# Performance work log

Measured on AMD Instinct MI355X. Metric: run time of the kernel, lower is better.

## Reference

```python
import jax, jax.numpy as jnp
import numpy as np

N, CIN, COUT, V, T, S = 32, 64, 128, 25, 300, 3  # batch, in/out channels, joints, frames, subsets
EPS = 1e-5  # torch BatchNorm2d default eps


def setup_inputs() -> dict:
    key = jax.random.key(0)
    ks = jax.random.split(key, 16)
    f = lambda i, shape, sc=1.0: jax.random.normal(ks[i], shape, jnp.float32) * sc
    return dict(
        x=f(0, (N, CIN, V, T)),            # forward arg: input features
        ada_A=f(1, (N, CIN, V, V), 0.1),   # forward arg: adaptive adjacency features
        PA=f(2, (S, V, V), 0.1),           # learned adjacency (adaptive=True)
        conv3_w=f(3, (S, COUT, CIN), 0.05),  # per-subset 1x1 conv weights
        conv3_b=f(4, (S, COUT), 0.01),
        ada_w=f(5, (S, COUT, CIN), 0.05),    # per-subset conv_ada weights
        ada_b=f(6, (S, COUT), 0.01),
        bn_gamma=jnp.ones((COUT,), jnp.float32),
        bn_beta=jnp.zeros((COUT,), jnp.float32),
        bn_mean=f(7, (COUT,), 0.01),
        bn_var=jnp.abs(f(8, (COUT,))) + 1.0,
        down_w=f(9, (COUT, CIN), 0.05),      # residual 1x1 conv (in_c != out_c)
        down_b=f(10, (COUT,), 0.01),
        dbn_gamma=jnp.ones((COUT,), jnp.float32),
        dbn_beta=jnp.zeros((COUT,), jnp.float32),
        dbn_mean=f(11, (COUT,), 0.01),
        dbn_var=jnp.abs(f(12, (COUT,))) + 1.0,
    )


def _bn(y, g, b, m, v):
    # inference-mode BatchNorm2d over channel axis 1; y: [N, C, V, T]
    scale = g * jax.lax.rsqrt(v + EPS)
    return (y - m[:, None, None]) * scale[:, None, None] + b[:, None, None]


def reference(x, ada_A, PA, conv3_w, conv3_b, ada_w, ada_b,
              bn_gamma, bn_beta, bn_mean, bn_var,
              down_w, down_b, dbn_gamma, dbn_beta, dbn_mean, dbn_var):
    # per-subset 1x1 conv on features: feat[s] = conv3_s(x)  -> [S, N, COUT, V, T]
    feat = jnp.einsum('nivt,soi->snovt', x, conv3_w) + conv3_b[:, None, :, None, None]
    # per-subset 1x1 conv on adjacency features -> [S, N, COUT, V, V]
    adaA = jnp.einsum('nivw,soi->snovw', ada_A, ada_w) + ada_b[:, None, :, None, None]
    # modulate by learned adjacency PA[s] broadcast over (batch, channel)
    A_full = adaA * PA[:, None, None, :, :]
    # graph matmul per subset + sum over subsets -> [N, COUT, V, T]
    out = jnp.einsum('snovw,snowt->novt', A_full, feat)
    out = _bn(out, bn_gamma, bn_beta, bn_mean, bn_var)
    # residual down-path: 1x1 conv + BN (in_c != out_c)
    res = jnp.einsum('nivt,oi->novt', x, down_w) + down_b[:, None, None]
    res = _bn(res, dbn_gamma, dbn_beta, dbn_mean, dbn_var)
    return jax.nn.relu(out + res)
```

## Files before the change

kernel.cpp:

```cpp
#include <hip/hip_runtime.h>
#include <stdint.h>

#define N_    32
#define CIN_  64
#define COUT_ 128
#define V_    25
#define T_    300
#define S_    3


using short8 = __attribute__((ext_vector_type(8))) short;
using f32x4  = __attribute__((ext_vector_type(4))) float;

#define MFMA(a, b, c) __builtin_amdgcn_mfma_f32_16x16x32_bf16(a, b, c, 0, 0, 0)

#define OC  8
#define TC  32

__device__ __forceinline__ float b2f(unsigned short u) {
  return __uint_as_float(((uint32_t)u) << 16);
}
__device__ __forceinline__ unsigned short f2b(float f) {
  uint32_t u = __float_as_uint(f);
  u += 0x7fffu + ((u >> 16) & 1u);
  return (unsigned short)(u >> 16);
}
template<bool ISB>
__device__ __forceinline__ float ldf(const void* p, int i) {
  return ISB ? b2f(((const unsigned short*)p)[i]) : ((const float*)p)[i];
}
__device__ __forceinline__ short8 zero8() {
  short8 z = {0, 0, 0, 0, 0, 0, 0, 0};
  return z;
}
__device__ __forceinline__ short8 ld_s8(const unsigned short* p, int st) {
  union { uint32_t u[4]; short8 s; } r;
  r.u[0] = (uint32_t)p[0]      | ((uint32_t)p[st]     << 16);
  r.u[1] = (uint32_t)p[2 * st] | ((uint32_t)p[3 * st] << 16);
  r.u[2] = (uint32_t)p[4 * st] | ((uint32_t)p[5 * st] << 16);
  r.u[3] = (uint32_t)p[6 * st] | ((uint32_t)p[7 * st] << 16);
  return r.s;
}
__device__ __forceinline__ short8 ld_f8h(const float* p, int st) {
  short8 r;
#pragma unroll
  for (int j = 0; j < 8; ++j) r[j] = (short)f2b(p[j * st]);
  return r;
}
__device__ __forceinline__ void ld_f8s(const float* p, int st,
                                       short8& h, short8& l) {
#pragma unroll
  for (int j = 0; j < 8; ++j) {
    float xv = p[j * st];
    uint32_t u = __float_as_uint(xv);
    h[j] = (short)(u >> 16);
    l[j] = (short)f2b(xv - __uint_as_float(u & 0xffff0000u));
  }
}

__global__ void gcn_dtype_flag(const void* __restrict__ gamma, int* __restrict__ flag) {
  if (threadIdx.x == 0 && blockIdx.x == 0)
    flag[0] = (((const unsigned short*)gamma)[0] == 0x3F80u) ? 1 : 0;
}

template<bool ISB>
__global__ __launch_bounds__(256) void gcn_mfma(
    const void* __restrict__ x,    const void* __restrict__ ada,
    const void* __restrict__ PA,
    const void* __restrict__ c3w,  const void* __restrict__ c3b,
    const void* __restrict__ adw,  const void* __restrict__ adb,
    const void* __restrict__ bng,  const void* __restrict__ bnb,
    const void* __restrict__ bnm,  const void* __restrict__ bnv,
    const void* __restrict__ dww,  const void* __restrict__ dwb,
    const void* __restrict__ dbg,  const void* __restrict__ dbb,
    const void* __restrict__ dbm,  const void* __restrict__ dbv,
    void* __restrict__ out,
    const int* __restrict__ flag)
{
  if (ISB) { if (flag && flag[0] == 0) return; }
  else     { if (!flag || flag[0] != 0) return; }

  __shared__ __align__(16) unsigned char SM[74752];
  unsigned short* A_l = (unsigned short*)SM;
  float* resl = (float*)(SM + 49152);

  const int tid  = threadIdx.x;
  const int lane = tid & 63;
  const int tl   = lane & 15;
  const int khi  = lane >> 4;
  const int wv   = tid >> 6;

  const int b  = blockIdx.x;
  const int q  = b >> 3;
  const int n  = (b & 7) * 4 + (q >> 4);
  const int o0 = (q & 15) * OC;

  const unsigned short* xnu   = (const unsigned short*)x   + (size_t)n * (CIN_ * V_ * T_);
  const float*          xnf   = (const float*)x            + (size_t)n * (CIN_ * V_ * T_);
  const unsigned short* adanu = (const unsigned short*)ada + (size_t)n * (CIN_ * V_ * V_);
  const float*          adanf = (const float*)ada          + (size_t)n * (CIN_ * V_ * V_);

  float sc8[OC];
#pragma unroll
  for (int o = 0; o < OC; ++o)
    sc8[o] = ldf<ISB>(bng, o0 + o) * rsqrtf(ldf<ISB>(bnv, o0 + o) + 1e-5f);

  const int oA = wv * 2, oB = wv * 2 + 1;
  const float dscA = ldf<ISB>(dbg, o0 + oA) * rsqrtf(ldf<ISB>(dbv, o0 + oA) + 1e-5f);
  const float dscB = ldf<ISB>(dbg, o0 + oB) * rsqrtf(ldf<ISB>(dbv, o0 + oB) + 1e-5f);
  const float c0A  = ldf<ISB>(bnb, o0 + oA) + ldf<ISB>(dbb, o0 + oA)
                   - ldf<ISB>(bnm, o0 + oA) * sc8[oA] - ldf<ISB>(dbm, o0 + oA) * dscA;
  const float c0B  = ldf<ISB>(bnb, o0 + oB) + ldf<ISB>(dbb, o0 + oB)
                   - ldf<ISB>(bnm, o0 + oB) * sc8[oB] - ldf<ISB>(dbm, o0 + oB) * dscB;

  const int r0 = tl;
  const int r1 = 16 + tl;
  short8 wb00, wb01, wb10, wb11;
  short8 wb00l = zero8(), wb01l = zero8(), wb10l = zero8(), wb11l = zero8();
  if constexpr (ISB) {
    const unsigned short* wrow0 = (const unsigned short*)c3w
        + ((r0 >> 3) * COUT_ + o0 + (r0 & 7)) * CIN_;
    const unsigned short* wrow1 = (r1 < 24)
        ? (const unsigned short*)c3w + (2 * COUT_ + o0 + (r1 & 7)) * CIN_
        : (const unsigned short*)dww + (o0 + (r1 & 7)) * CIN_;
    wb00 = *(const short8*)(wrow0 + khi * 8);
    wb01 = *(const short8*)(wrow0 + 32 + khi * 8);
    wb10 = *(const short8*)(wrow1 + khi * 8);
    wb11 = *(const short8*)(wrow1 + 32 + khi * 8);
  } else {
    const float* wrow0 = (const float*)c3w
        + ((r0 >> 3) * COUT_ + o0 + (r0 & 7)) * CIN_;
    const float* wrow1 = (r1 < 24)
        ? (const float*)c3w + (2 * COUT_ + o0 + (r1 & 7)) * CIN_
        : (const float*)dww + (o0 + (r1 & 7)) * CIN_;
    ld_f8s(wrow0 + khi * 8,      1, wb00, wb00l);
    ld_f8s(wrow0 + 32 + khi * 8, 1, wb01, wb01l);
    ld_f8s(wrow1 + khi * 8,      1, wb10, wb10l);
    ld_f8s(wrow1 + 32 + khi * 8, 1, wb11, wb11l);
  }

  f32x4 fb0, fb1;
#pragma unroll
  for (int rg = 0; rg < 4; ++rg) {
    const int ra = khi * 4 + rg;
    fb0[rg] = ldf<ISB>(c3b, (ra >> 3) * COUT_ + o0 + (ra & 7));
    const int rb = 16 + ra;
    fb1[rg] = (rb < 24) ? ldf<ISB>(c3b, 2 * COUT_ + o0 + (rb & 7))
                        : ldf<ISB>(dwb, o0 + (rb & 7));
  }

  for (int e = tid; e < 12288; e += 256) ((float*)SM)[e] = 0.f;
  __syncthreads();

  {
    short8 aw00, aw01, aw10, aw11;
    if constexpr (ISB) {
      const unsigned short* arow0 = (const unsigned short*)adw
          + ((r0 >> 3) * COUT_ + o0 + (r0 & 7)) * CIN_;
      const unsigned short* arow1 = (const unsigned short*)adw
          + (2 * COUT_ + o0 + (tl & 7)) * CIN_;
      aw00 = *(const short8*)(arow0 + khi * 8);
      aw01 = *(const short8*)(arow0 + 32 + khi * 8);
      aw10 = (tl < 8) ? *(const short8*)(arow1 + khi * 8)      : zero8();
      aw11 = (tl < 8) ? *(const short8*)(arow1 + 32 + khi * 8) : zero8();
    } else {
      const float* arow0 = (const float*)adw
          + ((r0 >> 3) * COUT_ + o0 + (r0 & 7)) * CIN_;
      const float* arow1 = (const float*)adw
          + (2 * COUT_ + o0 + (tl & 7)) * CIN_;
      aw00 = ld_f8h(arow0 + khi * 8, 1);
      aw01 = ld_f8h(arow0 + 32 + khi * 8, 1);
      aw10 = (tl < 8) ? ld_f8h(arow1 + khi * 8, 1)      : zero8();
      aw11 = (tl < 8) ? ld_f8h(arow1 + 32 + khi * 8, 1) : zero8();
    }
    f32x4 ab0, ab1;
#pragma unroll
    for (int rg = 0; rg < 4; ++rg) {
      const int ra = khi * 4 + rg;
      ab0[rg] = ldf<ISB>(adb, (ra >> 3) * COUT_ + o0 + (ra & 7));
      const int rb = 16 + ra;
      ab1[rg] = (rb < 24) ? ldf<ISB>(adb, 2 * COUT_ + o0 + (rb & 7)) : 0.f;
    }

    for (int nt = wv * 10; nt < wv * 10 + 10; ++nt) {
      const int pos = nt * 16 + tl;
      const bool pv = pos < V_ * V_;
      short8 bf0 = zero8(), bf1 = zero8();
      if (pv) {
        if constexpr (ISB) {
          bf0 = ld_s8(adanu + (khi * 8) * 625 + pos, 625);
          bf1 = ld_s8(adanu + (32 + khi * 8) * 625 + pos, 625);
        } else {
          bf0 = ld_f8h(adanf + (khi * 8) * 625 + pos, 625);
          bf1 = ld_f8h(adanf + (32 + khi * 8) * 625 + pos, 625);
        }
      }
      f32x4 a0 = ab0, a1 = ab1;
      a0 = MFMA(aw00, bf0, a0);
      a0 = MFMA(aw01, bf1, a0);
      a1 = MFMA(aw10, bf0, a1);
      a1 = MFMA(aw11, bf1, a1);
      if (pv) {
        const int vv = pos / 25, ww = pos % 25;
        const float pa0 = ldf<ISB>(PA, pos);
        const float pa1 = ldf<ISB>(PA, 625 + pos);
        const float pa2 = ldf<ISB>(PA, 1250 + pos);
#pragma unroll
        for (int rg = 0; rg < 4; ++rg) {
          const int ra = khi * 4 + rg;
          const float pa = (ra >> 3) ? pa1 : pa0;
          A_l[(((ra & 7) * 3 + (ra >> 3)) * 32 + vv) * 32 + ww] =
              f2b(a0[rg] * pa * sc8[ra & 7]);
          const int rb = 16 + ra;
          if (rb < 24)
            A_l[(((rb & 7) * 3 + 2) * 32 + vv) * 32 + ww] =
                f2b(a1[rg] * pa2 * sc8[rb & 7]);
        }
      }
    }
  }
  __syncthreads();

  short8 afr[2][3][2];
#pragma unroll
  for (int oc = 0; oc < 2; ++oc) {
    const int oo = wv * 2 + oc;
#pragma unroll
    for (int s = 0; s < 3; ++s)
#pragma unroll
      for (int mt = 0; mt < 2; ++mt)
        afr[oc][s][mt] = *(const short8*)(
            A_l + (((oo * 3 + s) * 32 + mt * 16 + tl) * 32 + khi * 8));
  }
  __syncthreads();

  for (int e = tid; e < 12288; e += 256) ((float*)SM)[e] = 0.f;
  __syncthreads();

  const int wlo = (wv == 0) ? 0 : 1 + 6 * wv;
  const int whi = 7 + 6 * wv;

  for (int ch = 0; ch < 10; ++ch) {
    const int t0 = ch * TC;

    for (int w = wlo; w < whi; ++w) {
#pragma unroll
      for (int nt = 0; nt < 2; ++nt) {
        const int tt = t0 + nt * 16;
        if (tt < T_) {
          const int t = tt + tl;
          f32x4 f0 = fb0, f1 = fb1;
          if constexpr (ISB) {
            short8 xf0 = zero8(), xf1 = zero8();
            if (t < T_) {
              const unsigned short* xp = xnu + (khi * 8) * (V_ * T_) + w * T_ + t;
              xf0 = ld_s8(xp, V_ * T_);
              xf1 = ld_s8(xp + 32 * (V_ * T_), V_ * T_);
            }
            f0 = MFMA(wb00, xf0, f0);
            f0 = MFMA(wb01, xf1, f0);
            f1 = MFMA(wb10, xf0, f1);
            f1 = MFMA(wb11, xf1, f1);
          } else {
            short8 xh0 = zero8(), xl0 = zero8(), xh1 = zero8(), xl1 = zero8();
            if (t < T_) {
              const float* xp = xnf + (khi * 8) * (V_ * T_) + w * T_ + t;
              ld_f8s(xp, V_ * T_, xh0, xl0);
              ld_f8s(xp + 32 * (V_ * T_), V_ * T_, xh1, xl1);
            }
            f32x4 g0 = {0.f, 0.f, 0.f, 0.f}, g1 = {0.f, 0.f, 0.f, 0.f};
            f0 = MFMA(wb00, xh0, f0);
            f0 = MFMA(wb01, xh1, f0);
            f1 = MFMA(wb10, xh0, f1);
            f1 = MFMA(wb11, xh1, f1);
            g0 = MFMA(wb00, xl0, g0);
            g0 = MFMA(wb01, xl1, g0);
            g0 = MFMA(wb00l, xh0, g0);
            g0 = MFMA(wb01l, xh1, g0);
            g1 = MFMA(wb10, xl0, g1);
            g1 = MFMA(wb11, xl1, g1);
            g1 = MFMA(wb10l, xh0, g1);
            g1 = MFMA(wb11l, xh1, g1);
            f0 = f0 + g0;
            f1 = f1 + g1;
          }
          const int tlc = nt * 16 + tl;
          const unsigned sw = (unsigned)(w * 2) ^ ((unsigned)(tlc & 3) << 4);
#pragma unroll
          for (int rg = 0; rg < 4; ++rg) {
            const int ra = khi * 4 + rg;
            *(unsigned short*)(SM + (ra * TC + tlc) * 64 + sw) = f2b(f0[rg]);
            const int rb = 16 + ra;
            if (rb < 24)
              *(unsigned short*)(SM + (rb * TC + tlc) * 64 + sw) = f2b(f1[rg]);
            else
              resl[((rb - 24) * V_ + w) * TC + tlc] = f1[rg];
          }
        }
      }
    }
    __syncthreads();

#pragma unroll
    for (int oc = 0; oc < 2; ++oc) {
      const int oo  = wv * 2 + oc;
      const float dsc = oc ? dscB : dscA;
      const float c0v = oc ? c0B : c0A;
#pragma unroll
      for (int nt = 0; nt < 2; ++nt) {
        const int tt = t0 + nt * 16;
        if (tt < T_) {
          const int tlc = nt * 16 + tl;
          const unsigned rsw = (unsigned)(khi ^ (tlc & 3)) << 4;
          f32x4 d0 = {0.f, 0.f, 0.f, 0.f};
          f32x4 d1 = {0.f, 0.f, 0.f, 0.f};
#pragma unroll
          for (int s = 0; s < 3; ++s) {
            const short8 bf =
                *(const short8*)(SM + ((s * 8 + oo) * TC + tlc) * 64 + rsw);
            d0 = MFMA(afr[oc][s][0], bf, d0);
            d1 = MFMA(afr[oc][s][1], bf, d1);
          }
          const int t = tt + tl;
          if (t < T_) {
            const size_t obase = (size_t)(n * COUT_ + o0 + oo) * (V_ * T_) + t;
            unsigned short* opu = (unsigned short*)out + obase;
            float*          opf = (float*)out + obase;
#pragma unroll
            for (int rg = 0; rg < 4; ++rg) {
              const int v0 = khi * 4 + rg;
              const float y0 = fmaxf(
                  d0[rg] + resl[(oo * V_ + v0) * TC + tlc] * dsc + c0v, 0.f);
              if constexpr (ISB) opu[v0 * T_] = f2b(y0);
              else               opf[v0 * T_] = y0;
              const int v1 = 16 + v0;
              if (v1 < V_) {
                const float y1 = fmaxf(
                    d1[rg] + resl[(oo * V_ + v1) * TC + tlc] * dsc + c0v, 0.f);
                if constexpr (ISB) opu[v1 * T_] = f2b(y1);
                else               opf[v1 * T_] = y1;
              }
            }
          }
        }
      }
    }
    __syncthreads();
  }
}

extern "C" void kernel_launch(void* const* d_in, const int* in_sizes, int n_in,
                              void* d_out, int out_size, void* d_ws, size_t ws_size,
                              hipStream_t stream) {
  int* flag = (ws_size >= sizeof(int)) ? (int*)d_ws : nullptr;
  if (flag) gcn_dtype_flag<<<1, 64, 0, stream>>>(d_in[7], flag);

  gcn_mfma<true><<<dim3(512), 256, 0, stream>>>(
      d_in[0], d_in[1], d_in[2], d_in[3], d_in[4], d_in[5], d_in[6],
      d_in[7], d_in[8], d_in[9], d_in[10], d_in[11], d_in[12],
      d_in[13], d_in[14], d_in[15], d_in[16], d_out, flag);

  if (flag)
    gcn_mfma<false><<<dim3(512), 256, 0, stream>>>(
        d_in[0], d_in[1], d_in[2], d_in[3], d_in[4], d_in[5], d_in[6],
        d_in[7], d_in[8], d_in[9], d_in[10], d_in[11], d_in[12],
        d_in[13], d_in[14], d_in[15], d_in[16], d_out, flag);
}
```

Before: 453.2 us.

## Split time axis across blocks, shrink LDS, and prepack fp32 x into bf16 hi/lo pairs

Grid doubles to 1024 blocks, each covering half the time range in 16-frame chunks. This shrinks LDS from ~73KB to ~38KB and adds launch_bounds occupancy 4, so more blocks fit per CU. A new pack_x pre-pass converts fp32 x into packed bf16 hi/lo words in the workspace, so the main kernel loads one 32-bit word per element instead of splitting floats in-loop. The A buffer layout is trimmed to 25 rows with a new LDS swizzle. The trade-offs are that the graph-adjacency prologue is recomputed twice as often and the extra pack pass adds global traffic.

```diff
diff --git a/kernel.cpp b/kernel.cpp
--- a/kernel.cpp
+++ b/kernel.cpp
@@ -14,8 +14,8 @@
 
 #define MFMA(a, b, c) __builtin_amdgcn_mfma_f32_16x16x32_bf16(a, b, c, 0, 0, 0)
 
-#define OC  8
-#define TC  32
+#define OC   8
+#define TCH  16
 
 __device__ __forceinline__ float b2f(unsigned short u) {
   return __uint_as_float(((uint32_t)u) << 16);
@@ -57,14 +57,56 @@
     l[j] = (short)f2b(xv - __uint_as_float(u & 0xffff0000u));
   }
 }
+__device__ __forceinline__ void ld_pk8(const uint32_t* p, int st,
+                                       short8& h, short8& l) {
+  uint32_t a[8];
+#pragma unroll
+  for (int j = 0; j < 8; ++j) a[j] = p[j * st];
+  union { uint32_t u[4]; short8 s; } H, L;
+#pragma unroll
+  for (int k = 0; k < 4; ++k) {
+    H.u[k] = (a[2 * k] >> 16)      | (a[2 * k + 1] & 0xffff0000u);
+    L.u[k] = (a[2 * k] & 0xffffu)  | (a[2 * k + 1] << 16);
+  }
+  h = H.s; l = L.s;
+}
 
 __global__ void gcn_dtype_flag(const void* __restrict__ gamma, int* __restrict__ flag) {
   if (threadIdx.x == 0 && blockIdx.x == 0)
     flag[0] = (((const unsigned short*)gamma)[0] == 0x3F80u) ? 1 : 0;
 }
 
-template<bool ISB>
-__global__ __launch_bounds__(256) void gcn_mfma(
+__global__ __launch_bounds__(256) void pack_x(
+    const float* __restrict__ x, uint32_t* __restrict__ xp,
+    const int* __restrict__ flag) {
+  if (!flag || flag[0] != 0) return;
+  const int i = blockIdx.x * 256 + threadIdx.x;
+  const float4* s = (const float4*)x;
+  float4 a = s[2 * i], b = s[2 * i + 1];
+  uint4 o0, o1;
+  float av[4] = {a.x, a.y, a.z, a.w};
+  float bv[4] = {b.x, b.y, b.z, b.w};
+  uint32_t ou[8];
+#pragma unroll
+  for (int k = 0; k < 4; ++k) {
+    uint32_t u = __float_as_uint(av[k]);
+    uint32_t h = u & 0xffff0000u;
+    ou[k] = h | (uint32_t)f2b(av[k] - __uint_as_float(h));
+  }
+#pragma unroll
+  for (int k = 0; k < 4; ++k) {
+    uint32_t u = __float_as_uint(bv[k]);
+    uint32_t h = u & 0xffff0000u;
+    ou[4 + k] = h | (uint32_t)f2b(bv[k] - __uint_as_float(h));
+  }
+  o0.x = ou[0]; o0.y = ou[1]; o0.z = ou[2]; o0.w = ou[3];
+  o1.x = ou[4]; o1.y = ou[5]; o1.z = ou[6]; o1.w = ou[7];
+  ((uint4*)xp)[2 * i]     = o0;
+  ((uint4*)xp)[2 * i + 1] = o1;
+}
+
+template<bool ISB, bool PACK>
+__global__ __launch_bounds__(256, 4) void gcn_mfma(
     const void* __restrict__ x,    const void* __restrict__ ada,
     const void* __restrict__ PA,
     const void* __restrict__ c3w,  const void* __restrict__ c3b,
@@ -75,14 +117,15 @@
     const void* __restrict__ dbg,  const void* __restrict__ dbb,
     const void* __restrict__ dbm,  const void* __restrict__ dbv,
     void* __restrict__ out,
+    const uint32_t* __restrict__ xpk,
     const int* __restrict__ flag)
 {
   if (ISB) { if (flag && flag[0] == 0) return; }
   else     { if (!flag || flag[0] != 0) return; }
 
-  __shared__ __align__(16) unsigned char SM[74752];
+  __shared__ __align__(16) unsigned char SM[38400];
   unsigned short* A_l = (unsigned short*)SM;
-  float* resl = (float*)(SM + 49152);
+  float* resl = (float*)(SM + 24576);
 
   const int tid  = threadIdx.x;
   const int lane = tid & 63;
@@ -92,11 +135,15 @@
 
   const int b  = blockIdx.x;
   const int q  = b >> 3;
-  const int n  = (b & 7) * 4 + (q >> 4);
-  const int o0 = (q & 15) * OC;
+  const int n  = (b & 7) * 4 + (q >> 5);
+  const int o0 = ((q >> 1) & 15) * OC;
+  const int th = q & 1;
+  const int tbase = th ? 160 : 0;
+  const int nch   = th ? 9 : 10;
 
   const unsigned short* xnu   = (const unsigned short*)x   + (size_t)n * (CIN_ * V_ * T_);
   const float*          xnf   = (const float*)x            + (size_t)n * (CIN_ * V_ * T_);
+  const uint32_t*       xnq   = xpk                        + (size_t)n * (CIN_ * V_ * T_);
   const unsigned short* adanu = (const unsigned short*)ada + (size_t)n * (CIN_ * V_ * V_);
   const float*          adanf = (const float*)ada          + (size_t)n * (CIN_ * V_ * V_);
 
@@ -149,7 +196,7 @@
                         : ldf<ISB>(dwb, o0 + (rb & 7));
   }
 
-  for (int e = tid; e < 12288; e += 256) ((float*)SM)[e] = 0.f;
+  for (int e = tid; e < 9600; e += 256) ((float*)SM)[e] = 0.f;
   __syncthreads();
 
   {
@@ -209,11 +256,11 @@
         for (int rg = 0; rg < 4; ++rg) {
           const int ra = khi * 4 + rg;
           const float pa = (ra >> 3) ? pa1 : pa0;
-          A_l[(((ra & 7) * 3 + (ra >> 3)) * 32 + vv) * 32 + ww] =
+          A_l[(((ra & 7) * 3 + (ra >> 3)) * 25 + vv) * 32 + ww] =
               f2b(a0[rg] * pa * sc8[ra & 7]);
           const int rb = 16 + ra;
           if (rb < 24)
-            A_l[(((rb & 7) * 3 + 2) * 32 + vv) * 32 + ww] =
+            A_l[(((rb & 7) * 3 + 2) * 25 + vv) * 32 + ww] =
                 f2b(a1[rg] * pa2 * sc8[rb & 7]);
         }
       }
@@ -226,77 +273,77 @@
   for (int oc = 0; oc < 2; ++oc) {
     const int oo = wv * 2 + oc;
 #pragma unroll
-    for (int s = 0; s < 3; ++s)
-#pragma unroll
-      for (int mt = 0; mt < 2; ++mt)
-        afr[oc][s][mt] = *(const short8*)(
-            A_l + (((oo * 3 + s) * 32 + mt * 16 + tl) * 32 + khi * 8));
+    for (int s = 0; s < 3; ++s) {
+      afr[oc][s][0] = *(const short8*)(
+          A_l + (((oo * 3 + s) * 25 + tl) * 32 + khi * 8));
+      afr[oc][s][1] = (tl < 9)
+          ? *(const short8*)(A_l + (((oo * 3 + s) * 25 + 16 + tl) * 32 + khi * 8))
+          : zero8();
+    }
   }
   __syncthreads();
 
-  for (int e = tid; e < 12288; e += 256) ((float*)SM)[e] = 0.f;
+  for (int e = tid; e < 6144; e += 256) ((float*)SM)[e] = 0.f;
   __syncthreads();
 
   const int wlo = (wv == 0) ? 0 : 1 + 6 * wv;
   const int whi = 7 + 6 * wv;
 
-  for (int ch = 0; ch < 10; ++ch) {
-    const int t0 = ch * TC;
+  for (int ch = 0; ch < nch; ++ch) {
+    const int t  = tbase + ch * TCH + tl;
+    const bool tv = t < T_;
 
     for (int w = wlo; w < whi; ++w) {
-#pragma unroll
-      for (int nt = 0; nt < 2; ++nt) {
-        const int tt = t0 + nt * 16;
-        if (tt < T_) {
-          const int t = tt + tl;
-          f32x4 f0 = fb0, f1 = fb1;
-          if constexpr (ISB) {
-            short8 xf0 = zero8(), xf1 = zero8();
-            if (t < T_) {
-              const unsigned short* xp = xnu + (khi * 8) * (V_ * T_) + w * T_ + t;
-              xf0 = ld_s8(xp, V_ * T_);
-              xf1 = ld_s8(xp + 32 * (V_ * T_), V_ * T_);
-            }
-            f0 = MFMA(wb00, xf0, f0);
-            f0 = MFMA(wb01, xf1, f0);
-            f1 = MFMA(wb10, xf0, f1);
-            f1 = MFMA(wb11, xf1, f1);
+      f32x4 f0 = fb0, f1 = fb1;
+      if constexpr (ISB) {
+        short8 xf0 = zero8(), xf1 = zero8();
+        if (tv) {
+          const unsigned short* xp = xnu + (khi * 8) * (V_ * T_) + w * T_ + t;
+          xf0 = ld_s8(xp, V_ * T_);
+          xf1 = ld_s8(xp + 32 * (V_ * T_), V_ * T_);
+        }
+        f0 = MFMA(wb00, xf0, f0);
+        f0 = MFMA(wb01, xf1, f0);
+        f1 = MFMA(wb10, xf0, f1);
+        f1 = MFMA(wb11, xf1, f1);
+      } else {
+        short8 xh0 = zero8(), xl0 = zero8(), xh1 = zero8(), xl1 = zero8();
+        if (tv) {
+          const int off = (khi * 8) * (V_ * T_) + w * T_ + t;
+          if constexpr (PACK) {
+            ld_pk8(xnq + off, V_ * T_, xh0, xl0);
+            ld_pk8(xnq + off + 32 * (V_ * T_), V_ * T_, xh1, xl1);
           } else {
-            short8 xh0 = zero8(), xl0 = zero8(), xh1 = zero8(), xl1 = zero8();
-            if (t < T_) {
-              const float* xp = xnf + (khi * 8) * (V_ * T_) + w * T_ + t;
-              ld_f8s(xp, V_ * T_, xh0, xl0);
-              ld_f8s(xp + 32 * (V_ * T_), V_ * T_, xh1, xl1);
-            }
-            f32x4 g0 = {0.f, 0.f, 0.f, 0.f}, g1 = {0.f, 0.f, 0.f, 0.f};
-            f0 = MFMA(wb00, xh0, f0);
-            f0 = MFMA(wb01, xh1, f0);
-            f1 = MFMA(wb10, xh0, f1);
-            f1 = MFMA(wb11, xh1, f1);
-            g0 = MFMA(wb00, xl0, g0);
-            g0 = MFMA(wb01, xl1, g0);
-            g0 = MFMA(wb00l, xh0, g0);
-            g0 = MFMA(wb01l, xh1, g0);
-            g1 = MFMA(wb10, xl0, g1);
-            g1 = MFMA(wb11, xl1, g1);
-            g1 = MFMA(wb10l, xh0, g1);
-            g1 = MFMA(wb11l, xh1, g1);
-            f0 = f0 + g0;
-            f1 = f1 + g1;
-          }
-          const int tlc = nt * 16 + tl;
-          const unsigned sw = (unsigned)(w * 2) ^ ((unsigned)(tlc & 3) << 4);
-#pragma unroll
-          for (int rg = 0; rg < 4; ++rg) {
-            const int ra = khi * 4 + rg;
-            *(unsigned short*)(SM + (ra * TC + tlc) * 64 + sw) = f2b(f0[rg]);
-            const int rb = 16 + ra;
-            if (rb < 24)
-              *(unsigned short*)(SM + (rb * TC + tlc) * 64 + sw) = f2b(f1[rg]);
-            else
-              resl[((rb - 24) * V_ + w) * TC + tlc] = f1[rg];
+            ld_f8s(xnf + off, V_ * T_, xh0, xl0);
+            ld_f8s(xnf + off + 32 * (V_ * T_), V_ * T_, xh1, xl1);
           }
         }
+        f32x4 g0 = {0.f, 0.f, 0.f, 0.f}, g1 = {0.f, 0.f, 0.f, 0.f};
+        f0 = MFMA(wb00, xh0, f0);
+        f0 = MFMA(wb01, xh1, f0);
+        f1 = MFMA(wb10, xh0, f1);
+        f1 = MFMA(wb11, xh1, f1);
+        g0 = MFMA(wb00, xl0, g0);
+        g0 = MFMA(wb01, xl1, g0);
+        g0 = MFMA(wb00l, xh0, g0);
+        g0 = MFMA(wb01l, xh1, g0);
+        g1 = MFMA(wb10, xl0, g1);
+        g1 = MFMA(wb11, xl1, g1);
+        g1 = MFMA(wb10l, xh0, g1);
+        g1 = MFMA(wb11l, xh1, g1);
+        f0 = f0 + g0;
+        f1 = f1 + g1;
+      }
+      const int swb = ((((w >> 3) ^ (tl & 3) ^ khi) & 3) << 4) + (w & 7) * 2;
+#pragma unroll
+      for (int rg = 0; rg < 4; ++rg) {
+        const int ra = khi * 4 + rg;
+        *(unsigned short*)(SM + ra * 1024 + tl * 64 + swb) = f2b(f0[rg]);
+        const int rb = 16 + ra;
+        if (rb < 24)
+          *(unsigned short*)(SM + rb * 1024 + tl * 64 + swb) = f2b(f1[rg]);
+        else
+          resl[((khi * 4 + rg - 8) * 25 + w) * 16 + tl] = f1[rg];
       }
     }
     __syncthreads();
@@ -306,41 +353,34 @@
       const int oo  = wv * 2 + oc;
       const float dsc = oc ? dscB : dscA;
       const float c0v = oc ? c0B : c0A;
-#pragma unroll
-      for (int nt = 0; nt < 2; ++nt) {
-        const int tt = t0 + nt * 16;
-        if (tt < T_) {
-          const int tlc = nt * 16 + tl;
-          const unsigned rsw = (unsigned)(khi ^ (tlc & 3)) << 4;
-          f32x4 d0 = {0.f, 0.f, 0.f, 0.f};
-          f32x4 d1 = {0.f, 0.f, 0.f, 0.f};
-#pragma unroll
-          for (int s = 0; s < 3; ++s) {
-            const short8 bf =
-                *(const short8*)(SM + ((s * 8 + oo) * TC + tlc) * 64 + rsw);
-            d0 = MFMA(afr[oc][s][0], bf, d0);
-            d1 = MFMA(afr[oc][s][1], bf, d1);
-          }
-          const int t = tt + tl;
-          if (t < T_) {
-            const size_t obase = (size_t)(n * COUT_ + o0 + oo) * (V_ * T_) + t;
-            unsigned short* opu = (unsigned short*)out + obase;
-            float*          opf = (float*)out + obase;
-#pragma unroll
-            for (int rg = 0; rg < 4; ++rg) {
-              const int v0 = khi * 4 + rg;
-              const float y0 = fmaxf(
-                  d0[rg] + resl[(oo * V_ + v0) * TC + tlc] * dsc + c0v, 0.f);
-              if constexpr (ISB) opu[v0 * T_] = f2b(y0);
-              else               opf[v0 * T_] = y0;
-              const int v1 = 16 + v0;
-              if (v1 < V_) {
-                const float y1 = fmaxf(
-                    d1[rg] + resl[(oo * V_ + v1) * TC + tlc] * dsc + c0v, 0.f);
-                if constexpr (ISB) opu[v1 * T_] = f2b(y1);
-                else               opf[v1 * T_] = y1;
-              }
-            }
+      f32x4 d0 = {0.f, 0.f, 0.f, 0.f};
+      f32x4 d1 = {0.f, 0.f, 0.f, 0.f};
+#pragma unroll
+      for (int s = 0; s < 3; ++s) {
+        const int row = s * 8 + oo;
+        const short8 bf = *(const short8*)(
+            SM + row * 1024 + tl * 64
+               + (((khi ^ (tl & 3) ^ ((row >> 2) & 3)) & 3) << 4));
+        d0 = MFMA(afr[oc][s][0], bf, d0);
+        d1 = MFMA(afr[oc][s][1], bf, d1);
+      }
+      if (tv) {
+        const size_t obase = (size_t)(n * COUT_ + o0 + oo) * (V_ * T_) + t;
+        unsigned short* opu = (unsigned short*)out + obase;
+        float*          opf = (float*)out + obase;
+#pragma unroll
+        for (int rg = 0; rg < 4; ++rg) {
+          const int v0 = khi * 4 + rg;
+          const float y0 = fmaxf(
+              d0[rg] + resl[(oo * 25 + v0) * 16 + tl] * dsc + c0v, 0.f);
+          if constexpr (ISB) opu[v0 * T_] = f2b(y0);
+          else               opf[v0 * T_] = y0;
+          const int v1 = 16 + v0;
+          if (v1 < V_) {
+            const float y1 = fmaxf(
+                d1[rg] + resl[(oo * 25 + v1) * 16 + tl] * dsc + c0v, 0.f);
+            if constexpr (ISB) opu[v1 * T_] = f2b(y1);
+            else               opf[v1 * T_] = y1;
           }
         }
       }
@@ -352,17 +392,29 @@
 extern "C" void kernel_launch(void* const* d_in, const int* in_sizes, int n_in,
                               void* d_out, int out_size, void* d_ws, size_t ws_size,
                               hipStream_t stream) {
+  const size_t XPK_OFF   = 1024;
+  const size_t XPK_BYTES = (size_t)N_ * CIN_ * V_ * T_ * 4;
   int* flag = (ws_size >= sizeof(int)) ? (int*)d_ws : nullptr;
+  const bool ws_ok = flag && ws_size >= XPK_OFF + XPK_BYTES;
+  uint32_t* xpk = ws_ok ? (uint32_t*)((char*)d_ws + XPK_OFF) : nullptr;
+
   if (flag) gcn_dtype_flag<<<1, 64, 0, stream>>>(d_in[7], flag);
-
-  gcn_mfma<true><<<dim3(512), 256, 0, stream>>>(
+  if (ws_ok)
+    pack_x<<<dim3(7500), 256, 0, stream>>>((const float*)d_in[0], xpk, flag);
+
+  gcn_mfma<true, false><<<dim3(1024), 256, 0, stream>>>(
       d_in[0], d_in[1], d_in[2], d_in[3], d_in[4], d_in[5], d_in[6],
       d_in[7], d_in[8], d_in[9], d_in[10], d_in[11], d_in[12],
-      d_in[13], d_in[14], d_in[15], d_in[16], d_out, flag);
-
-  if (flag)
-    gcn_mfma<false><<<dim3(512), 256, 0, stream>>>(
+      d_in[13], d_in[14], d_in[15], d_in[16], d_out, nullptr, flag);
+
+  if (ws_ok)
+    gcn_mfma<false, true><<<dim3(1024), 256, 0, stream>>>(
         d_in[0], d_in[1], d_in[2], d_in[3], d_in[4], d_in[5], d_in[6],
         d_in[7], d_in[8], d_in[9], d_in[10], d_in[11], d_in[12],
-        d_in[13], d_in[14], d_in[15], d_in[16], d_out, flag);
-}
+        d_in[13], d_in[14], d_in[15], d_in[16], d_out, xpk, flag);
+  else if (flag)
+    gcn_mfma<false, false><<<dim3(1024), 256, 0, stream>>>(
+        d_in[0], d_in[1], d_in[2], d_in[3], d_in[4], d_in[5], d_in[6],
+        d_in[7], d_in[8], d_in[9], d_in[10], d_in[11], d_in[12],
+        d_in[13], d_in[14], d_in[15], d_in[16], d_out, nullptr, flag);
+}
```

Measured after the change: 479.4 us. +5.8%, slower.

## Pre-transpose x to channel-contiguous layout and halve per-block output channels

Applied to the files above, without the earlier changes.

Adds pre-pass kernels that transpose x into a [n][v][t][cin] bf16 layout in workspace (for fp32 input, split into hi/lo bf16 planes), so the main kernel can load MFMA B fragments with 16-byte vector loads instead of strided 2-byte gathers. The main kernel now handles 4 output channels per block over 1024 blocks with less shared memory and a 4-blocks-per-CU launch bound, and processes two joints per iteration in the bf16 path. This removes uncoalesced strided loads and raises occupancy, at the cost of an extra transpose pass and workspace traffic. The fp32 hi/lo split is changed to round-to-nearest.

```diff
diff --git a/kernel.cpp b/kernel.cpp
--- a/kernel.cpp
+++ b/kernel.cpp
@@ -13,9 +13,6 @@
 using f32x4  = __attribute__((ext_vector_type(4))) float;
 
 #define MFMA(a, b, c) __builtin_amdgcn_mfma_f32_16x16x32_bf16(a, b, c, 0, 0, 0)
-
-#define OC  8
-#define TC  32
 
 __device__ __forceinline__ float b2f(unsigned short u) {
   return __uint_as_float(((uint32_t)u) << 16);
@@ -52,9 +49,9 @@
 #pragma unroll
   for (int j = 0; j < 8; ++j) {
     float xv = p[j * st];
-    uint32_t u = __float_as_uint(xv);
-    h[j] = (short)(u >> 16);
-    l[j] = (short)f2b(xv - __uint_as_float(u & 0xffff0000u));
+    unsigned short hu = f2b(xv);
+    h[j] = (short)hu;
+    l[j] = (short)f2b(xv - b2f(hu));
   }
 }
 
@@ -63,8 +60,69 @@
     flag[0] = (((const unsigned short*)gamma)[0] == 0x3F80u) ? 1 : 0;
 }
 
-template<bool ISB>
-__global__ __launch_bounds__(256) void gcn_mfma(
+__global__ __launch_bounds__(256) void tx_bf(
+    const unsigned short* __restrict__ x, unsigned short* __restrict__ xt,
+    const int* __restrict__ flag) {
+  if (!flag || flag[0] == 0) return;
+  __shared__ uint32_t til[64][151];
+  const int b = blockIdx.x, n = b / 25, v = b % 25, tid = threadIdx.x;
+  const unsigned short* xp = x + (size_t)n * 480000 + v * 300;
+  for (int u = tid; u < 9600; u += 256) {
+    const int i = u / 150, tp = u % 150;
+    til[i][tp] = *(const uint32_t*)(xp + (size_t)i * 7500 + 2 * tp);
+  }
+  __syncthreads();
+  unsigned short* op = xt + (size_t)n * 480000 + (size_t)v * 19200;
+  for (int u = tid; u < 2400; u += 256) {
+    const int t = u >> 3, oct = u & 7;
+    uint32_t pk[4];
+#pragma unroll
+    for (int j = 0; j < 4; ++j) {
+      const uint32_t w0 = til[oct * 8 + 2 * j][t >> 1];
+      const uint32_t w1 = til[oct * 8 + 2 * j + 1][t >> 1];
+      const uint32_t a = (t & 1) ? (w0 >> 16) : (w0 & 0xffffu);
+      const uint32_t c = (t & 1) ? (w1 >> 16) : (w1 & 0xffffu);
+      pk[j] = a | (c << 16);
+    }
+    *(uint4*)(op + t * 64 + oct * 8) = *(uint4*)pk;
+  }
+}
+
+__global__ __launch_bounds__(256) void tx_f32(
+    const float* __restrict__ x, unsigned short* __restrict__ xh,
+    unsigned short* __restrict__ xl, const int* __restrict__ flag) {
+  if (!flag || flag[0] != 0) return;
+  __shared__ uint32_t til[64][303];
+  const int b = blockIdx.x, n = b / 25, v = b % 25, tid = threadIdx.x;
+  const float* xp = x + (size_t)n * 480000 + v * 300;
+  for (int u = tid; u < 9600; u += 256) {
+    const int i = u / 150, tp = u % 150;
+    const float2 xv = *(const float2*)(xp + (size_t)i * 7500 + 2 * tp);
+    unsigned short h0 = f2b(xv.x), h1 = f2b(xv.y);
+    unsigned short l0 = f2b(xv.x - b2f(h0)), l1 = f2b(xv.y - b2f(h1));
+    til[i][2 * tp]     = ((uint32_t)h0 << 16) | l0;
+    til[i][2 * tp + 1] = ((uint32_t)h1 << 16) | l1;
+  }
+  __syncthreads();
+  const size_t ob = (size_t)n * 480000 + (size_t)v * 19200;
+  for (int u = tid; u < 2400; u += 256) {
+    const int t = u >> 3, oct = u & 7;
+    uint32_t w[8];
+#pragma unroll
+    for (int k = 0; k < 8; ++k) w[k] = til[oct * 8 + k][t];
+    uint32_t ph[4], pl[4];
+#pragma unroll
+    for (int j = 0; j < 4; ++j) {
+      ph[j] = (w[2 * j] >> 16) | (w[2 * j + 1] & 0xffff0000u);
+      pl[j] = (w[2 * j] & 0xffffu) | (w[2 * j + 1] << 16);
+    }
+    *(uint4*)(xh + ob + t * 64 + oct * 8) = *(uint4*)ph;
+    *(uint4*)(xl + ob + t * 64 + oct * 8) = *(uint4*)pl;
+  }
+}
+
+template<bool ISB, bool TR>
+__global__ __launch_bounds__(256, 4) void gcn_mfma(
     const void* __restrict__ x,    const void* __restrict__ ada,
     const void* __restrict__ PA,
     const void* __restrict__ c3w,  const void* __restrict__ c3b,
@@ -75,14 +133,16 @@
     const void* __restrict__ dbg,  const void* __restrict__ dbb,
     const void* __restrict__ dbm,  const void* __restrict__ dbv,
     void* __restrict__ out,
+    const unsigned short* __restrict__ xt0,
+    const unsigned short* __restrict__ xt1,
     const int* __restrict__ flag)
 {
   if (ISB) { if (flag && flag[0] == 0) return; }
   else     { if (!flag || flag[0] != 0) return; }
 
-  __shared__ __align__(16) unsigned char SM[74752];
+  __shared__ __align__(16) unsigned char SM[37776];
   unsigned short* A_l = (unsigned short*)SM;
-  float* resl = (float*)(SM + 49152);
+  float* resl = (float*)(SM + 24576);
 
   const int tid  = threadIdx.x;
   const int lane = tid & 63;
@@ -91,100 +151,69 @@
   const int wv   = tid >> 6;
 
   const int b  = blockIdx.x;
-  const int q  = b >> 3;
-  const int n  = (b & 7) * 4 + (q >> 4);
-  const int o0 = (q & 15) * OC;
-
-  const unsigned short* xnu   = (const unsigned short*)x   + (size_t)n * (CIN_ * V_ * T_);
-  const float*          xnf   = (const float*)x            + (size_t)n * (CIN_ * V_ * T_);
-  const unsigned short* adanu = (const unsigned short*)ada + (size_t)n * (CIN_ * V_ * V_);
-  const float*          adanf = (const float*)ada          + (size_t)n * (CIN_ * V_ * V_);
-
-  float sc8[OC];
-#pragma unroll
-  for (int o = 0; o < OC; ++o)
-    sc8[o] = ldf<ISB>(bng, o0 + o) * rsqrtf(ldf<ISB>(bnv, o0 + o) + 1e-5f);
-
-  const int oA = wv * 2, oB = wv * 2 + 1;
-  const float dscA = ldf<ISB>(dbg, o0 + oA) * rsqrtf(ldf<ISB>(dbv, o0 + oA) + 1e-5f);
-  const float dscB = ldf<ISB>(dbg, o0 + oB) * rsqrtf(ldf<ISB>(dbv, o0 + oB) + 1e-5f);
-  const float c0A  = ldf<ISB>(bnb, o0 + oA) + ldf<ISB>(dbb, o0 + oA)
-                   - ldf<ISB>(bnm, o0 + oA) * sc8[oA] - ldf<ISB>(dbm, o0 + oA) * dscA;
-  const float c0B  = ldf<ISB>(bnb, o0 + oB) + ldf<ISB>(dbb, o0 + oB)
-                   - ldf<ISB>(bnm, o0 + oB) * sc8[oB] - ldf<ISB>(dbm, o0 + oB) * dscB;
-
-  const int r0 = tl;
-  const int r1 = 16 + tl;
-  short8 wb00, wb01, wb10, wb11;
-  short8 wb00l = zero8(), wb01l = zero8(), wb10l = zero8(), wb11l = zero8();
+  const int n  = (b & 7) * 4 + (b >> 8);
+  const int o0 = ((b >> 3) & 31) * 4;
+
+  const unsigned short* xnu   = (const unsigned short*)x   + (size_t)n * 480000;
+  const float*          xnf   = (const float*)x            + (size_t)n * 480000;
+  const unsigned short* adanu = (const unsigned short*)ada + (size_t)n * 40000;
+  const float*          adanf = (const float*)ada          + (size_t)n * 40000;
+  const unsigned short* xtn   = xt0 ? xt0 + (size_t)n * 480000 : nullptr;
+  const unsigned short* xln   = xt1 ? xt1 + (size_t)n * 480000 : nullptr;
+
+  float sc4[4];
+#pragma unroll
+  for (int o = 0; o < 4; ++o)
+    sc4[o] = ldf<ISB>(bng, o0 + o) * rsqrtf(ldf<ISB>(bnv, o0 + o) + 1e-5f);
+  const float dscv = ldf<ISB>(dbg, o0 + wv) * rsqrtf(ldf<ISB>(dbv, o0 + wv) + 1e-5f);
+  const float c0v  = ldf<ISB>(bnb, o0 + wv) + ldf<ISB>(dbb, o0 + wv)
+                   - ldf<ISB>(bnm, o0 + wv) * sc4[wv] - ldf<ISB>(dbm, o0 + wv) * dscv;
+
+  short8 wb0, wb1, wb0l = zero8(), wb1l = zero8();
   if constexpr (ISB) {
-    const unsigned short* wrow0 = (const unsigned short*)c3w
-        + ((r0 >> 3) * COUT_ + o0 + (r0 & 7)) * CIN_;
-    const unsigned short* wrow1 = (r1 < 24)
-        ? (const unsigned short*)c3w + (2 * COUT_ + o0 + (r1 & 7)) * CIN_
-        : (const unsigned short*)dww + (o0 + (r1 & 7)) * CIN_;
-    wb00 = *(const short8*)(wrow0 + khi * 8);
-    wb01 = *(const short8*)(wrow0 + 32 + khi * 8);
-    wb10 = *(const short8*)(wrow1 + khi * 8);
-    wb11 = *(const short8*)(wrow1 + 32 + khi * 8);
+    const unsigned short* wr = (tl < 12)
+        ? (const unsigned short*)c3w + ((tl >> 2) * COUT_ + o0 + (tl & 3)) * CIN_
+        : (const unsigned short*)dww + (o0 + (tl & 3)) * CIN_;
+    wb0 = *(const short8*)(wr + khi * 8);
+    wb1 = *(const short8*)(wr + 32 + khi * 8);
   } else {
-    const float* wrow0 = (const float*)c3w
-        + ((r0 >> 3) * COUT_ + o0 + (r0 & 7)) * CIN_;
-    const float* wrow1 = (r1 < 24)
-        ? (const float*)c3w + (2 * COUT_ + o0 + (r1 & 7)) * CIN_
-        : (const float*)dww + (o0 + (r1 & 7)) * CIN_;
-    ld_f8s(wrow0 + khi * 8,      1, wb00, wb00l);
-    ld_f8s(wrow0 + 32 + khi * 8, 1, wb01, wb01l);
-    ld_f8s(wrow1 + khi * 8,      1, wb10, wb10l);
-    ld_f8s(wrow1 + 32 + khi * 8, 1, wb11, wb11l);
-  }
-
-  f32x4 fb0, fb1;
-#pragma unroll
-  for (int rg = 0; rg < 4; ++rg) {
-    const int ra = khi * 4 + rg;
-    fb0[rg] = ldf<ISB>(c3b, (ra >> 3) * COUT_ + o0 + (ra & 7));
-    const int rb = 16 + ra;
-    fb1[rg] = (rb < 24) ? ldf<ISB>(c3b, 2 * COUT_ + o0 + (rb & 7))
-                        : ldf<ISB>(dwb, o0 + (rb & 7));
-  }
-
-  for (int e = tid; e < 12288; e += 256) ((float*)SM)[e] = 0.f;
-  __syncthreads();
-
+    const float* wr = (tl < 12)
+        ? (const float*)c3w + ((tl >> 2) * COUT_ + o0 + (tl & 3)) * CIN_
+        : (const float*)dww + (o0 + (tl & 3)) * CIN_;
+    ld_f8s(wr + khi * 8,      1, wb0, wb0l);
+    ld_f8s(wr + 32 + khi * 8, 1, wb1, wb1l);
+  }
+  f32x4 fbias;
+#pragma unroll
+  for (int rg = 0; rg < 4; ++rg)
+    fbias[rg] = (khi < 3) ? ldf<ISB>(c3b, khi * COUT_ + o0 + rg)
+                          : ldf<ISB>(dwb, o0 + rg);
+
+  for (int e = tid; e < 4800; e += 256) ((float*)SM)[e] = 0.f;
+  __syncthreads();
   {
-    short8 aw00, aw01, aw10, aw11;
-    if constexpr (ISB) {
-      const unsigned short* arow0 = (const unsigned short*)adw
-          + ((r0 >> 3) * COUT_ + o0 + (r0 & 7)) * CIN_;
-      const unsigned short* arow1 = (const unsigned short*)adw
-          + (2 * COUT_ + o0 + (tl & 7)) * CIN_;
-      aw00 = *(const short8*)(arow0 + khi * 8);
-      aw01 = *(const short8*)(arow0 + 32 + khi * 8);
-      aw10 = (tl < 8) ? *(const short8*)(arow1 + khi * 8)      : zero8();
-      aw11 = (tl < 8) ? *(const short8*)(arow1 + 32 + khi * 8) : zero8();
-    } else {
-      const float* arow0 = (const float*)adw
-          + ((r0 >> 3) * COUT_ + o0 + (r0 & 7)) * CIN_;
-      const float* arow1 = (const float*)adw
-          + (2 * COUT_ + o0 + (tl & 7)) * CIN_;
-      aw00 = ld_f8h(arow0 + khi * 8, 1);
-      aw01 = ld_f8h(arow0 + 32 + khi * 8, 1);
-      aw10 = (tl < 8) ? ld_f8h(arow1 + khi * 8, 1)      : zero8();
-      aw11 = (tl < 8) ? ld_f8h(arow1 + 32 + khi * 8, 1) : zero8();
-    }
-    f32x4 ab0, ab1;
-#pragma unroll
-    for (int rg = 0; rg < 4; ++rg) {
-      const int ra = khi * 4 + rg;
-      ab0[rg] = ldf<ISB>(adb, (ra >> 3) * COUT_ + o0 + (ra & 7));
-      const int rb = 16 + ra;
-      ab1[rg] = (rb < 24) ? ldf<ISB>(adb, 2 * COUT_ + o0 + (rb & 7)) : 0.f;
-    }
-
-    for (int nt = wv * 10; nt < wv * 10 + 10; ++nt) {
-      const int pos = nt * 16 + tl;
-      const bool pv = pos < V_ * V_;
+    short8 aw0 = zero8(), aw1 = zero8();
+    if (tl < 12) {
+      if constexpr (ISB) {
+        const unsigned short* ar = (const unsigned short*)adw
+            + ((tl >> 2) * COUT_ + o0 + (tl & 3)) * CIN_;
+        aw0 = *(const short8*)(ar + khi * 8);
+        aw1 = *(const short8*)(ar + 32 + khi * 8);
+      } else {
+        const float* ar = (const float*)adw
+            + ((tl >> 2) * COUT_ + o0 + (tl & 3)) * CIN_;
+        aw0 = ld_f8h(ar + khi * 8, 1);
+        aw1 = ld_f8h(ar + 32 + khi * 8, 1);
+      }
+    }
+    f32x4 ab;
+#pragma unroll
+    for (int rg = 0; rg < 4; ++rg)
+      ab[rg] = (khi < 3) ? ldf<ISB>(adb, khi * COUT_ + o0 + rg) : 0.f;
+
+    for (int ti = wv * 10; ti < wv * 10 + 10; ++ti) {
+      const int pos = ti * 16 + tl;
+      const bool pv = pos < 625;
       short8 bf0 = zero8(), bf1 = zero8();
       if (pv) {
         if constexpr (ISB) {
@@ -195,153 +224,167 @@
           bf1 = ld_f8h(adanf + (32 + khi * 8) * 625 + pos, 625);
         }
       }
-      f32x4 a0 = ab0, a1 = ab1;
-      a0 = MFMA(aw00, bf0, a0);
-      a0 = MFMA(aw01, bf1, a0);
-      a1 = MFMA(aw10, bf0, a1);
-      a1 = MFMA(aw11, bf1, a1);
-      if (pv) {
+      f32x4 acc = ab;
+      acc = MFMA(aw0, bf0, acc);
+      acc = MFMA(aw1, bf1, acc);
+      if (pv && khi < 3) {
         const int vv = pos / 25, ww = pos % 25;
-        const float pa0 = ldf<ISB>(PA, pos);
-        const float pa1 = ldf<ISB>(PA, 625 + pos);
-        const float pa2 = ldf<ISB>(PA, 1250 + pos);
-#pragma unroll
-        for (int rg = 0; rg < 4; ++rg) {
-          const int ra = khi * 4 + rg;
-          const float pa = (ra >> 3) ? pa1 : pa0;
-          A_l[(((ra & 7) * 3 + (ra >> 3)) * 32 + vv) * 32 + ww] =
-              f2b(a0[rg] * pa * sc8[ra & 7]);
-          const int rb = 16 + ra;
-          if (rb < 24)
-            A_l[(((rb & 7) * 3 + 2) * 32 + vv) * 32 + ww] =
-                f2b(a1[rg] * pa2 * sc8[rb & 7]);
-        }
-      }
-    }
-  }
-  __syncthreads();
-
-  short8 afr[2][3][2];
-#pragma unroll
-  for (int oc = 0; oc < 2; ++oc) {
-    const int oo = wv * 2 + oc;
-#pragma unroll
-    for (int s = 0; s < 3; ++s)
-#pragma unroll
-      for (int mt = 0; mt < 2; ++mt)
-        afr[oc][s][mt] = *(const short8*)(
-            A_l + (((oo * 3 + s) * 32 + mt * 16 + tl) * 32 + khi * 8));
-  }
-  __syncthreads();
-
-  for (int e = tid; e < 12288; e += 256) ((float*)SM)[e] = 0.f;
-  __syncthreads();
-
-  const int wlo = (wv == 0) ? 0 : 1 + 6 * wv;
-  const int whi = 7 + 6 * wv;
+        const float pa = ldf<ISB>(PA, khi * 625 + pos);
+#pragma unroll
+        for (int rg = 0; rg < 4; ++rg)
+          A_l[((rg * 3 + khi) * 25 + vv) * 32 + ww] = f2b(acc[rg] * pa * sc4[rg]);
+      }
+    }
+  }
+  __syncthreads();
+
+  short8 afr[3][2];
+#pragma unroll
+  for (int s = 0; s < 3; ++s) {
+    afr[s][0] = *(const short8*)(A_l + ((wv * 3 + s) * 25 + tl) * 32 + khi * 8);
+    afr[s][1] = (tl < 9)
+        ? *(const short8*)(A_l + ((wv * 3 + s) * 25 + 16 + tl) * 32 + khi * 8)
+        : zero8();
+  }
+  __syncthreads();
+
+  for (int e = tid; e < 6144; e += 256) ((float*)SM)[e] = 0.f;
+  __syncthreads();
+
+  const int wlo = wv * 6;
+  const int whi = (wv == 3) ? 25 : wv * 6 + 6;
 
   for (int ch = 0; ch < 10; ++ch) {
-    const int t0 = ch * TC;
-
-    for (int w = wlo; w < whi; ++w) {
-#pragma unroll
-      for (int nt = 0; nt < 2; ++nt) {
-        const int tt = t0 + nt * 16;
-        if (tt < T_) {
-          const int t = tt + tl;
-          f32x4 f0 = fb0, f1 = fb1;
-          if constexpr (ISB) {
-            short8 xf0 = zero8(), xf1 = zero8();
-            if (t < T_) {
-              const unsigned short* xp = xnu + (khi * 8) * (V_ * T_) + w * T_ + t;
-              xf0 = ld_s8(xp, V_ * T_);
-              xf1 = ld_s8(xp + 32 * (V_ * T_), V_ * T_);
-            }
-            f0 = MFMA(wb00, xf0, f0);
-            f0 = MFMA(wb01, xf1, f0);
-            f1 = MFMA(wb10, xf0, f1);
-            f1 = MFMA(wb11, xf1, f1);
-          } else {
-            short8 xh0 = zero8(), xl0 = zero8(), xh1 = zero8(), xl1 = zero8();
-            if (t < T_) {
-              const float* xp = xnf + (khi * 8) * (V_ * T_) + w * T_ + t;
-              ld_f8s(xp, V_ * T_, xh0, xl0);
-              ld_f8s(xp + 32 * (V_ * T_), V_ * T_, xh1, xl1);
-            }
-            f32x4 g0 = {0.f, 0.f, 0.f, 0.f}, g1 = {0.f, 0.f, 0.f, 0.f};
-            f0 = MFMA(wb00, xh0, f0);
-            f0 = MFMA(wb01, xh1, f0);
-            f1 = MFMA(wb10, xh0, f1);
-            f1 = MFMA(wb11, xh1, f1);
-            g0 = MFMA(wb00, xl0, g0);
-            g0 = MFMA(wb01, xl1, g0);
-            g0 = MFMA(wb00l, xh0, g0);
-            g0 = MFMA(wb01l, xh1, g0);
-            g1 = MFMA(wb10, xl0, g1);
-            g1 = MFMA(wb11, xl1, g1);
-            g1 = MFMA(wb10l, xh0, g1);
-            g1 = MFMA(wb11l, xh1, g1);
-            f0 = f0 + g0;
-            f1 = f1 + g1;
-          }
+    const int t0 = ch * 32;
+
+    if constexpr (ISB) {
+      for (int w = wlo; w < whi; w += 2) {
+        const bool pr = (w + 1 < whi);
+#pragma unroll
+        for (int nt = 0; nt < 2; ++nt) {
           const int tlc = nt * 16 + tl;
-          const unsigned sw = (unsigned)(w * 2) ^ ((unsigned)(tlc & 3) << 4);
-#pragma unroll
-          for (int rg = 0; rg < 4; ++rg) {
-            const int ra = khi * 4 + rg;
-            *(unsigned short*)(SM + (ra * TC + tlc) * 64 + sw) = f2b(f0[rg]);
-            const int rb = 16 + ra;
-            if (rb < 24)
-              *(unsigned short*)(SM + (rb * TC + tlc) * 64 + sw) = f2b(f1[rg]);
-            else
-              resl[((rb - 24) * V_ + w) * TC + tlc] = f1[rg];
-          }
-        }
-      }
-    }
-    __syncthreads();
-
-#pragma unroll
-    for (int oc = 0; oc < 2; ++oc) {
-      const int oo  = wv * 2 + oc;
-      const float dsc = oc ? dscB : dscA;
-      const float c0v = oc ? c0B : c0A;
-#pragma unroll
-      for (int nt = 0; nt < 2; ++nt) {
-        const int tt = t0 + nt * 16;
-        if (tt < T_) {
-          const int tlc = nt * 16 + tl;
-          const unsigned rsw = (unsigned)(khi ^ (tlc & 3)) << 4;
-          f32x4 d0 = {0.f, 0.f, 0.f, 0.f};
-          f32x4 d1 = {0.f, 0.f, 0.f, 0.f};
-#pragma unroll
-          for (int s = 0; s < 3; ++s) {
-            const short8 bf =
-                *(const short8*)(SM + ((s * 8 + oo) * TC + tlc) * 64 + rsw);
-            d0 = MFMA(afr[oc][s][0], bf, d0);
-            d1 = MFMA(afr[oc][s][1], bf, d1);
-          }
-          const int t = tt + tl;
-          if (t < T_) {
-            const size_t obase = (size_t)(n * COUT_ + o0 + oo) * (V_ * T_) + t;
-            unsigned short* opu = (unsigned short*)out + obase;
-            float*          opf = (float*)out + obase;
-#pragma unroll
-            for (int rg = 0; rg < 4; ++rg) {
-              const int v0 = khi * 4 + rg;
-              const float y0 = fmaxf(
-                  d0[rg] + resl[(oo * V_ + v0) * TC + tlc] * dsc + c0v, 0.f);
-              if constexpr (ISB) opu[v0 * T_] = f2b(y0);
-              else               opf[v0 * T_] = y0;
-              const int v1 = 16 + v0;
-              if (v1 < V_) {
-                const float y1 = fmaxf(
-                    d1[rg] + resl[(oo * V_ + v1) * TC + tlc] * dsc + c0v, 0.f);
-                if constexpr (ISB) opu[v1 * T_] = f2b(y1);
-                else               opf[v1 * T_] = y1;
+          const int t = t0 + tlc;
+          short8 a0 = zero8(), a1 = zero8(), b0 = zero8(), b1 = zero8();
+          if (t < 300) {
+            if constexpr (TR) {
+              const unsigned short* p = xtn + ((size_t)(w * 300 + t) << 6);
+              a0 = *(const short8*)(p + khi * 8);
+              a1 = *(const short8*)(p + 32 + khi * 8);
+              if (pr) {
+                b0 = *(const short8*)(p + 19200 + khi * 8);
+                b1 = *(const short8*)(p + 19200 + 32 + khi * 8);
+              }
+            } else {
+              const unsigned short* p = xnu + (khi * 8) * 7500 + w * 300 + t;
+              a0 = ld_s8(p, 7500);
+              a1 = ld_s8(p + 32 * 7500, 7500);
+              if (pr) {
+                b0 = ld_s8(p + 300, 7500);
+                b1 = ld_s8(p + 300 + 32 * 7500, 7500);
               }
             }
           }
+          f32x4 fA = fbias, fB = fbias;
+          fA = MFMA(wb0, a0, fA);
+          fA = MFMA(wb1, a1, fA);
+          fB = MFMA(wb0, b0, fB);
+          fB = MFMA(wb1, b1, fB);
+          if (khi == 3) {
+#pragma unroll
+            for (int rg = 0; rg < 4; ++rg) {
+              resl[(rg * 25 + w) * 33 + tlc] = fA[rg];
+              if (pr) resl[(rg * 25 + w + 1) * 33 + tlc] = fB[rg];
+            }
+          } else {
+            const int sb = ((((w >> 3) ^ (tl & 3) ^ khi) & 3) << 4) + (w & 7) * 2;
+            if (pr) {
+#pragma unroll
+              for (int rg = 0; rg < 4; ++rg)
+                *(uint32_t*)(SM + (khi * 4 + rg) * 2048 + tlc * 64 + sb)
+                    = (uint32_t)f2b(fA[rg]) | ((uint32_t)f2b(fB[rg]) << 16);
+            } else {
+#pragma unroll
+              for (int rg = 0; rg < 4; ++rg)
+                *(unsigned short*)(SM + (khi * 4 + rg) * 2048 + tlc * 64 + sb)
+                    = f2b(fA[rg]);
+            }
+          }
+        }
+      }
+    } else {
+      for (int w = wlo; w < whi; ++w) {
+#pragma unroll
+        for (int nt = 0; nt < 2; ++nt) {
+          const int tlc = nt * 16 + tl;
+          const int t = t0 + tlc;
+          short8 h0 = zero8(), h1 = zero8(), l0 = zero8(), l1 = zero8();
+          if (t < 300) {
+            if constexpr (TR) {
+              const size_t off = (size_t)(w * 300 + t) << 6;
+              h0 = *(const short8*)(xtn + off + khi * 8);
+              h1 = *(const short8*)(xtn + off + 32 + khi * 8);
+              l0 = *(const short8*)(xln + off + khi * 8);
+              l1 = *(const short8*)(xln + off + 32 + khi * 8);
+            } else {
+              const float* p = xnf + (khi * 8) * 7500 + w * 300 + t;
+              ld_f8s(p, 7500, h0, l0);
+              ld_f8s(p + 32 * 7500, 7500, h1, l1);
+            }
+          }
+          f32x4 f = fbias, g = {0.f, 0.f, 0.f, 0.f};
+          f = MFMA(wb0, h0, f);
+          f = MFMA(wb1, h1, f);
+          g = MFMA(wb0, l0, g);
+          g = MFMA(wb1, l1, g);
+          g = MFMA(wb0l, h0, g);
+          g = MFMA(wb1l, h1, g);
+          f = f + g;
+          if (khi == 3) {
+#pragma unroll
+            for (int rg = 0; rg < 4; ++rg)
+              resl[(rg * 25 + w) * 33 + tlc] = f[rg];
+          } else {
+            const int sb = ((((w >> 3) ^ (tl & 3) ^ khi) & 3) << 4) + (w & 7) * 2;
+#pragma unroll
+            for (int rg = 0; rg < 4; ++rg)
+              *(unsigned short*)(SM + (khi * 4 + rg) * 2048 + tlc * 64 + sb)
+                  = f2b(f[rg]);
+          }
+        }
+      }
+    }
+    __syncthreads();
+
+#pragma unroll
+    for (int nt = 0; nt < 2; ++nt) {
+      const int tlc = nt * 16 + tl;
+      const int t = t0 + tlc;
+      f32x4 d0 = {0.f, 0.f, 0.f, 0.f};
+      f32x4 d1 = {0.f, 0.f, 0.f, 0.f};
+#pragma unroll
+      for (int s = 0; s < 3; ++s) {
+        const int row = s * 4 + wv;
+        const short8 bf = *(const short8*)(
+            SM + row * 2048 + tlc * 64 + (((khi ^ (tlc & 3) ^ s) & 3) << 4));
+        d0 = MFMA(afr[s][0], bf, d0);
+        d1 = MFMA(afr[s][1], bf, d1);
+      }
+      if (t < 300) {
+        const int obase = (n * COUT_ + o0 + wv) * 7500 + t;
+#pragma unroll
+        for (int rg = 0; rg < 4; ++rg) {
+          const int v0 = khi * 4 + rg;
+          const float y0 = fmaxf(
+              d0[rg] + resl[(wv * 25 + v0) * 33 + tlc] * dscv + c0v, 0.f);
+          if constexpr (ISB) ((unsigned short*)out)[obase + v0 * 300] = f2b(y0);
+          else               ((float*)out)[obase + v0 * 300] = y0;
+          const int v1 = 16 + v0;
+          if (v1 < 25) {
+            const float y1 = fmaxf(
+                d1[rg] + resl[(wv * 25 + v1) * 33 + tlc] * dscv + c0v, 0.f);
+            if constexpr (ISB) ((unsigned short*)out)[obase + v1 * 300] = f2b(y1);
+            else               ((float*)out)[obase + v1 * 300] = y1;
+          }
         }
       }
     }
@@ -352,17 +395,40 @@
 extern "C" void kernel_launch(void* const* d_in, const int* in_sizes, int n_in,
                               void* d_out, int out_size, void* d_ws, size_t ws_size,
                               hipStream_t stream) {
+  const size_t PL = 30720000;
   int* flag = (ws_size >= sizeof(int)) ? (int*)d_ws : nullptr;
+  unsigned short* P0 = (unsigned short*)((char*)d_ws + 1024);
+  unsigned short* P1 = (unsigned short*)((char*)d_ws + 1024 + PL);
+  const bool trb = flag && ws_size >= 1024 + PL;
+  const bool trf = flag && ws_size >= 1024 + 2 * PL;
+
   if (flag) gcn_dtype_flag<<<1, 64, 0, stream>>>(d_in[7], flag);
-
-  gcn_mfma<true><<<dim3(512), 256, 0, stream>>>(
-      d_in[0], d_in[1], d_in[2], d_in[3], d_in[4], d_in[5], d_in[6],
-      d_in[7], d_in[8], d_in[9], d_in[10], d_in[11], d_in[12],
-      d_in[13], d_in[14], d_in[15], d_in[16], d_out, flag);
-
-  if (flag)
-    gcn_mfma<false><<<dim3(512), 256, 0, stream>>>(
+  if (trb) tx_bf<<<dim3(800), 256, 0, stream>>>(
+      (const unsigned short*)d_in[0], P0, flag);
+  if (trf) tx_f32<<<dim3(800), 256, 0, stream>>>(
+      (const float*)d_in[0], P0, P1, flag);
+
+  if (trb)
+    gcn_mfma<true, true><<<dim3(1024), 256, 0, stream>>>(
         d_in[0], d_in[1], d_in[2], d_in[3], d_in[4], d_in[5], d_in[6],
         d_in[7], d_in[8], d_in[9], d_in[10], d_in[11], d_in[12],
-        d_in[13], d_in[14], d_in[15], d_in[16], d_out, flag);
-}
+        d_in[13], d_in[14], d_in[15], d_in[16], d_out, P0, nullptr, flag);
+  else
+    gcn_mfma<true, false><<<dim3(1024), 256, 0, stream>>>(
+        d_in[0], d_in[1], d_in[2], d_in[3], d_in[4], d_in[5], d_in[6],
+        d_in[7], d_in[8], d_in[9], d_in[10], d_in[11], d_in[12],
+        d_in[13], d_in[14], d_in[15], d_in[16], d_out, nullptr, nullptr, flag);
+
+  if (flag) {
+    if (trf)
+      gcn_mfma<false, true><<<dim3(1024), 256, 0, stream>>>(
+          d_in[0], d_in[1], d_in[2], d_in[3], d_in[4], d_in[5], d_in[6],
+          d_in[7], d_in[8], d_in[9], d_in[10], d_in[11], d_in[12],
+          d_in[13], d_in[14], d_in[15], d_in[16], d_out, P0, P1, flag);
+    else
+      gcn_mfma<false, false><<<dim3(1024), 256, 0, stream>>>(
+          d_in[0], d_in[1], d_in[2], d_in[3], d_in[4], d_in[5], d_in[6],
+          d_in[7], d_in[8], d_in[9], d_in[10], d_in[11], d_in[12],
+          d_in[13], d_in[14], d_in[15], d_in[16], d_out, nullptr, nullptr, flag);
+  }
+}
```

After: 496.6 us. 9.6% more time.
